# Optimization experiments

Measured on AMD Instinct MI355X. Metric: run time of the kernel, lower is better.

## Reference

```python
import jax, jax.numpy as jnp
import numpy as np

B, D, H, T = 8192, 256, 266, 20  # batch, dim, dim+10, num timesteps
LAMBDA = 1.0
SIGMA = 1.0
EPS = 1e-5  # torch BatchNorm1d default eps


def _bn(h, g, b):
    # training-mode BatchNorm1d: biased batch statistics over axis 0
    m = h.mean(0)
    v = h.var(0)
    return g * (h - m) * jax.lax.rsqrt(v + EPS) + b


def _hidden(x, W, b, g, be):
    return jax.nn.relu(_bn(x @ W.T + b, g, be))


def setup_inputs() -> dict:
    key = jax.random.key(0)
    ks = jax.random.split(key, 16)

    def n(k, shape, s=0.05):
        return jax.random.normal(k, shape, jnp.float32) * s

    inp = {}
    inp["x"] = jax.random.normal(ks[0], (B, D), jnp.float32)
    inp["xi"] = jax.random.normal(ks[1], (T, B, D), jnp.float32)
    inp["timegrid"] = jnp.linspace(0.0, 1.0, T + 1).astype(jnp.float32)
    # per-timestep stacks of Linear+BN params (i_h1, h1_h2, h2_o)
    inp["W1"] = n(ks[2], (T, H, D)); inp["b1"] = jnp.zeros((T, H), jnp.float32)
    inp["g1"] = jnp.ones((T, H), jnp.float32); inp["be1"] = jnp.zeros((T, H), jnp.float32)
    inp["W2"] = n(ks[3], (T, H, H)); inp["b2"] = jnp.zeros((T, H), jnp.float32)
    inp["g2"] = jnp.ones((T, H), jnp.float32); inp["be2"] = jnp.zeros((T, H), jnp.float32)
    inp["W3"] = n(ks[4], (T, D, H)); inp["b3"] = jnp.zeros((T, D), jnp.float32)
    # v0 network: hiddenLayer(D,H) -> hiddenLayer(H,H) -> hiddenLayer(H,1)
    inp["vW1"] = n(ks[5], (H, D)); inp["vb1"] = jnp.zeros((H,), jnp.float32)
    inp["vg1"] = jnp.ones((H,), jnp.float32); inp["vbe1"] = jnp.zeros((H,), jnp.float32)
    inp["vW2"] = n(ks[6], (H, H)); inp["vb2"] = jnp.zeros((H,), jnp.float32)
    inp["vg2"] = jnp.ones((H,), jnp.float32); inp["vbe2"] = jnp.zeros((H,), jnp.float32)
    inp["vW3"] = n(ks[7], (1, H)); inp["vb3"] = jnp.zeros((1,), jnp.float32)
    inp["vg3"] = jnp.ones((1,), jnp.float32); inp["vbe3"] = jnp.zeros((1,), jnp.float32)
    return inp


def reference(x, xi, timegrid, W1, b1, g1, be1, W2, b2, g2, be2, W3, b3,
              vW1, vb1, vg1, vbe1, vW2, vb2, vg2, vbe2, vW3, vb3, vg3, vbe3):
    # v0 sub-network evaluated on the initial x (i == 0 branch)
    v0 = _hidden(x, vW1, vb1, vg1, vbe1)
    v0 = _hidden(v0, vW2, vb2, vg2, vbe2)
    v0 = _hidden(v0, vW3, vb3, vg3, vbe3)  # [B, 1]

    hsteps = timegrid[1:] - timegrid[:-1]  # [T]

    def step(carry, inp_t):
        xt, vt = carry
        (W1t, b1t, g1t, be1t, W2t, b2t, g2t, be2t, W3t, b3t, ht, xit) = inp_t
        h1 = _hidden(xt, W1t, b1t, g1t, be1t)
        h2 = _hidden(h1, W2t, b2t, g2t, be2t)
        grad = h2 @ W3t.T + b3t                     # [B, D]
        alpha = -jnp.sqrt(LAMBDA) * grad
        f = jnp.sum(alpha * alpha, axis=1)          # ||alpha||_2^2 per row
        noise = SIGMA * jnp.sqrt(ht) * xit          # sigma*sqrt(h)*xi
        # diag(grad @ noise.T) == row-wise dot product (same math, O(B*D))
        dot = jnp.sum(grad * noise, axis=1)
        vt = vt - (f * ht)[:, None] + dot[:, None]
        xt = xt + alpha * ht + noise
        return (xt, vt), None

    (xT, vT), _ = jax.lax.scan(
        step, (x, v0),
        (W1, b1, g1, be1, W2, b2, g2, be2, W3, b3, hsteps, xi))
    return vT, xT
```

## Files before the change

### kernel.cpp

```cpp
#include <hip/hip_runtime.h>
#include <hip/hip_bf16.h>
#include <math.h>

#define BATCH 8192
#define DDIM 256
#define HDIM 266
#define NPAD 320
#define TSTEPS 20
#define BN_EPS 1e-5f
#define LSTR 72
#define NBLK 256
#define NBAR 64

typedef __attribute__((ext_vector_type(8))) short short8;
typedef __attribute__((ext_vector_type(4))) float f32x4;

__device__ __forceinline__ short f2bf(float f) {
    __hip_bfloat16 h = __float2bfloat16(f);
    return *reinterpret_cast<short*>(&h);
}
__device__ __forceinline__ float bf2f(short s) {
    union { unsigned u; float f; } v;
    v.u = ((unsigned)(unsigned short)s) << 16;
    return v.f;
}

#define SZ_W1B (20L * 320 * 256)
#define SZ_W2B (20L * 320 * 320)
#define SZ_W3B (20L * 256 * 320)
#define SZ_VW1 (320L * 256)
#define SZ_VW2 (320L * 320)
#define SZ_B1P (20L * 320)
#define SZ_B2P (20L * 320)
#define ZCOUNT (4L * 21 * NPAD + 2 + NBAR)
#define PREP_TOTAL (SZ_W1B + SZ_W2B + SZ_W3B + SZ_VW1 + SZ_VW2 + SZ_B1P + SZ_B2P + 3 * 320 + ZCOUNT)

__global__ __launch_bounds__(256)
void prep_k(short* __restrict__ W1b, const float* __restrict__ W1,
            short* __restrict__ W2b, const float* __restrict__ W2,
            short* __restrict__ W3b, const float* __restrict__ W3,
            short* __restrict__ vW1b, const float* __restrict__ vW1,
            short* __restrict__ vW2b, const float* __restrict__ vW2,
            float* __restrict__ b1p, const float* __restrict__ b1,
            float* __restrict__ b2p, const float* __restrict__ b2,
            float* __restrict__ vb1p, const float* __restrict__ vb1,
            float* __restrict__ vb2p, const float* __restrict__ vb2,
            float* __restrict__ vW3p, const float* __restrict__ vW3,
            float* __restrict__ zbase)
{
    long idx = (long)blockIdx.x * 256 + threadIdx.x;
    if (idx < SZ_W1B) {
        long k = idx % 256, r = (idx / 256) % 320, t = idx / (256L * 320);
        float v = (r < HDIM) ? W1[((size_t)t * HDIM + r) * 256 + k] : 0.0f;
        W1b[idx] = f2bf(v); return;
    }
    idx -= SZ_W1B;
    if (idx < SZ_W2B) {
        long k = idx % 320, r = (idx / 320) % 320, t = idx / (320L * 320);
        float v = (r < HDIM && k < HDIM) ? W2[((size_t)t * HDIM + r) * HDIM + k] : 0.0f;
        W2b[idx] = f2bf(v); return;
    }
    idx -= SZ_W2B;
    if (idx < SZ_W3B) {
        long k = idx % 320, r = (idx / 320) % 256, t = idx / (320L * 256);
        float v = (k < HDIM) ? W3[((size_t)t * 256 + r) * HDIM + k] : 0.0f;
        W3b[idx] = f2bf(v); return;
    }
    idx -= SZ_W3B;
    if (idx < SZ_VW1) {
        long k = idx % 256, r = idx / 256;
        float v = (r < HDIM) ? vW1[(size_t)r * 256 + k] : 0.0f;
        vW1b[idx] = f2bf(v); return;
    }
    idx -= SZ_VW1;
    if (idx < SZ_VW2) {
        long k = idx % 320, r = idx / 320;
        float v = (r < HDIM && k < HDIM) ? vW2[(size_t)r * HDIM + k] : 0.0f;
        vW2b[idx] = f2bf(v); return;
    }
    idx -= SZ_VW2;
    if (idx < SZ_B1P) { long n = idx % 320, t = idx / 320;
        b1p[idx] = (n < HDIM) ? b1[(size_t)t * HDIM + n] : 0.0f; return; }
    idx -= SZ_B1P;
    if (idx < SZ_B2P) { long n = idx % 320, t = idx / 320;
        b2p[idx] = (n < HDIM) ? b2[(size_t)t * HDIM + n] : 0.0f; return; }
    idx -= SZ_B2P;
    if (idx < 320) { vb1p[idx] = (idx < HDIM) ? vb1[idx] : 0.0f; return; }
    idx -= 320;
    if (idx < 320) { vb2p[idx] = (idx < HDIM) ? vb2[idx] : 0.0f; return; }
    idx -= 320;
    if (idx < 320) { vW3p[idx] = (idx < HDIM) ? vW3[idx] : 0.0f; return; }
    idx -= 320;
    if (idx < ZCOUNT) { zbase[idx] = 0.0f; return; }
}

__device__ __forceinline__ void gridbar(unsigned* __restrict__ bar, int idx, int tid)
{
    asm volatile("s_waitcnt vmcnt(0) lgkmcnt(0)" ::: "memory");
    __syncthreads();
    if (tid == 0) {
        __hip_atomic_fetch_add(&bar[idx], 1u, __ATOMIC_RELAXED, __HIP_MEMORY_SCOPE_AGENT);
        while (__hip_atomic_load(&bar[idx], __ATOMIC_RELAXED, __HIP_MEMORY_SCOPE_AGENT)
               < (unsigned)NBLK) {
            __builtin_amdgcn_s_sleep(2);
        }
    }
    __syncthreads();
}

__device__ __forceinline__ float aload(const float* p)
{
    return __hip_atomic_load(p, __ATOMIC_RELAXED, __HIP_MEMORY_SCOPE_AGENT);
}

__device__ __forceinline__ void bn_coeff(const float* __restrict__ cs,
                                         const float* __restrict__ cq,
                                         const float* __restrict__ g,
                                         const float* __restrict__ be,
                                         float* sS, float* sT, int tid)
{
    for (int k = tid; k < NPAD; k += 512) {
        float s = 0.0f, t = 0.0f;
        if (k < HDIM) {
            float mn = aload(&cs[k]) * (1.0f / BATCH);
            float vr = aload(&cq[k]) * (1.0f / BATCH) - mn * mn;
            float rs = rsqrtf(fmaxf(vr, 0.0f) + BN_EPS);
            s = g[k] * rs;
            t = be[k] - mn * s;
        }
        sS[k] = s; sT[k] = t;
    }
}

template<int NJ>
__device__ __forceinline__ void preload_w(const short* __restrict__ Wt, int KLEN,
                                          short8* rW, int tid)
{
    #pragma unroll
    for (int i = 0; i < NJ; ++i) {
        int s = tid + 512 * i;
        rW[i] = *(const short8*)(Wt + (size_t)(s >> 3) * KLEN + ((s & 7) * 8));
    }
}

template<int NKT, int NJ, bool BN>
__device__ __forceinline__ void gemm_phase(
    const short* __restrict__ Wt, const short* Asrc, short* As1, short* Bs,
    const float* sS, const float* sT, f32x4* acc, short8* rW, int tid)
{
    const int lane = tid & 63, q = lane >> 4, m = lane & 15;
    const int w = tid >> 6, rh = w >> 2, ch = w & 3;
    const int srowA = tid >> 3, kqA = (tid & 7) * 8;
    const int KLEN = NKT * 64;

    #pragma unroll
    for (int kt = 0; kt < NKT; ++kt) {
        if (BN) {
            if (tid < 256) {
                short8 v = *(const short8*)&Asrc[(kt * 32 + srowA) * LSTR + kqA];
                short8 ta;
                #pragma unroll
                for (int j = 0; j < 8; ++j) {
                    int k = kt * 64 + kqA + j;
                    float f = bf2f(v[j]);
                    f = fmaxf(f * sS[k] + sT[k], 0.0f);
                    ta[j] = f2bf(f);
                }
                *(short8*)&As1[srowA * LSTR + kqA] = ta;
            }
        }
        #pragma unroll
        for (int i = 0; i < NJ; ++i) {
            int s = tid + 512 * i;
            *(short8*)&Bs[(s >> 3) * LSTR + (s & 7) * 8] = rW[i];
        }
        __syncthreads();
        if (kt < NKT - 1) {
            #pragma unroll
            for (int i = 0; i < NJ; ++i) {
                int s = tid + 512 * i;
                rW[i] = *(const short8*)(Wt + (size_t)(s >> 3) * KLEN
                                         + (kt + 1) * 64 + ((s & 7) * 8));
            }
        }
        const short* ab = BN ? As1 : (Asrc + kt * 32 * LSTR);
        #pragma unroll
        for (int kk = 0; kk < 2; ++kk) {
            short8 fa = *(const short8*)&ab[(rh * 16 + m) * LSTR + kk * 32 + q * 8];
            #pragma unroll
            for (int j = 0; j < NJ; ++j) {
                short8 fb = *(const short8*)&Bs[(ch * (NJ * 16) + j * 16 + m) * LSTR
                                                + kk * 32 + q * 8];
                acc[j] = __builtin_amdgcn_mfma_f32_16x16x32_bf16(fa, fb, acc[j], 0, 0, 0);
            }
        }
        __syncthreads();
    }
}

__device__ __forceinline__ void epi_store_stats(
    const f32x4* acc, const float* __restrict__ bias, short* dst,
    float* redS, float* redQ, float* __restrict__ csum, float* __restrict__ csq,
    int tid)
{
    const int lane = tid & 63, q = lane >> 4, m = lane & 15;
    const int w = tid >> 6, rh = w >> 2, ch = w & 3;
    float csv[5], cqv[5];
    #pragma unroll
    for (int j = 0; j < 5; ++j) {
        const int col = ch * 80 + j * 16 + m;
        const float bv = bias[col];
        float s = 0.0f, sq = 0.0f;
        #pragma unroll
        for (int r = 0; r < 4; ++r) {
            float v = acc[j][r] + bv;
            int row = rh * 16 + q * 4 + r;
            dst[((col >> 6) * 32 + row) * LSTR + (col & 63)] = f2bf(v);
            s += v; sq += v * v;
        }
        csv[j] = s; cqv[j] = sq;
    }
    #pragma unroll
    for (int j = 0; j < 5; ++j) {
        csv[j] += __shfl_xor(csv[j], 16); csv[j] += __shfl_xor(csv[j], 32);
        cqv[j] += __shfl_xor(cqv[j], 16); cqv[j] += __shfl_xor(cqv[j], 32);
    }
    if (q == 0) {
        #pragma unroll
        for (int j = 0; j < 5; ++j) {
            int col = ch * 80 + j * 16 + m;
            redS[rh * NPAD + col] = csv[j];
            redQ[rh * NPAD + col] = cqv[j];
        }
    }
    __syncthreads();
    if (tid < HDIM) {
        atomicAdd(&csum[tid], redS[tid] + redS[NPAD + tid]);
        atomicAdd(&csq[tid],  redQ[tid] + redQ[NPAD + tid]);
    }
}

struct PArgs {
    const float* x; const float* xi; const float* tg;
    const short* W1b; const short* W2b; const short* W3b;
    const short* vW1b; const short* vW2b;
    const float* b1p; const float* b2p; const float* b3;
    const float* vb1p; const float* vb2p; const float* vW3p; const float* vb3;
    const float* g1; const float* be1; const float* g2; const float* be2;
    const float* vg1; const float* vbe1; const float* vg2; const float* vbe2;
    const float* vg3; const float* vbe3;
    float* csA; float* cqA; float* csB; float* cqB;
    float* s3; float* q3;
    unsigned* bars;
    float* out; float* xout;
};

__global__ __launch_bounds__(512)
void persist_k(PArgs p)
{
    __shared__ __align__(16) short xbuf[128 * LSTR];
    __shared__ __align__(16) short h1buf[160 * LSTR];
    __shared__ __align__(16) short h2buf[160 * LSTR];
    __shared__ __align__(16) short Bs[320 * LSTR];
    __shared__ __align__(16) short As1[32 * LSTR];
    __shared__ float sS[NPAD], sT[NPAD];
    __shared__ float redS[2 * NPAD], redQ[2 * NPAD];
    __shared__ float redF[128], redD[128];
    __shared__ float pre3L[32], vacc[32];

    const int tid = threadIdx.x;
    const int row0 = blockIdx.x * 32;
    const int lane = tid & 63, w = tid >> 6, q = lane >> 4, m = lane & 15;
    const int rh = w >> 2, ch = w & 3;
    int bidx = 0;

    for (int i2 = tid; i2 < 32 * 256; i2 += 512) {
        int row = i2 >> 8, col = i2 & 255;
        xbuf[((col >> 6) * 32 + row) * LSTR + (col & 63)] =
            f2bf(p.x[(size_t)(row0 + row) * DDIM + col]);
    }
    if (tid < 32) vacc[tid] = 0.0f;

    short8 rW[5];
    f32x4 acc[5];

    preload_w<5>(p.vW1b, DDIM, rW, tid);
    #pragma unroll
    for (int j = 0; j < 5; ++j) acc[j] = (f32x4){0.f, 0.f, 0.f, 0.f};
    __syncthreads();
    gemm_phase<4, 5, false>(p.vW1b, xbuf, As1, Bs, sS, sT, acc, rW, tid);
    epi_store_stats(acc, p.vb1p, h1buf, redS, redQ,
                    p.csA + 20 * NPAD, p.cqA + 20 * NPAD, tid);
    preload_w<5>(p.vW2b, NPAD, rW, tid);
    gridbar(p.bars, bidx++, tid);

    bn_coeff(p.csA + 20 * NPAD, p.cqA + 20 * NPAD, p.vg1, p.vbe1, sS, sT, tid);
    #pragma unroll
    for (int j = 0; j < 5; ++j) acc[j] = (f32x4){0.f, 0.f, 0.f, 0.f};
    __syncthreads();
    gemm_phase<5, 5, true>(p.vW2b, h1buf, As1, Bs, sS, sT, acc, rW, tid);
    epi_store_stats(acc, p.vb2p, h2buf, redS, redQ,
                    p.csB + 20 * NPAD, p.cqB + 20 * NPAD, tid);
    gridbar(p.bars, bidx++, tid);

    bn_coeff(p.csB + 20 * NPAD, p.cqB + 20 * NPAD, p.vg2, p.vbe2, sS, sT, tid);
    __syncthreads();
    {
        const int wv = tid >> 6, ln = tid & 63;
        float ps = 0.0f, pq = 0.0f;
        #pragma unroll
        for (int r4 = 0; r4 < 4; ++r4) {
            int row = wv * 4 + r4;
            float sum = 0.0f;
            #pragma unroll
            for (int c = 0; c < 5; ++c) {
                int k = c * 64 + ln;
                float v = fmaxf(bf2f(h2buf[(c * 32 + row) * LSTR + ln]) * sS[k] + sT[k], 0.0f);
                sum += v * p.vW3p[k];
            }
            sum += __shfl_xor(sum, 1);  sum += __shfl_xor(sum, 2);
            sum += __shfl_xor(sum, 4);  sum += __shfl_xor(sum, 8);
            sum += __shfl_xor(sum, 16); sum += __shfl_xor(sum, 32);
            if (ln == 0) {
                float pv = sum + p.vb3[0];
                pre3L[row] = pv;
                ps += pv; pq += pv * pv;
            }
        }
        if (ln == 0) { redF[wv] = ps; redD[wv] = pq; }
        __syncthreads();
        if (tid == 0) {
            float a = 0.0f, b = 0.0f;
            #pragma unroll
            for (int i = 0; i < 8; ++i) { a += redF[i]; b += redD[i]; }
            atomicAdd(p.s3, a); atomicAdd(p.q3, b);
        }
    }

    for (int t = 0; t < TSTEPS; ++t) {
        preload_w<5>(p.W1b + (size_t)t * NPAD * DDIM, DDIM, rW, tid);
        #pragma unroll
        for (int j = 0; j < 5; ++j) acc[j] = (f32x4){0.f, 0.f, 0.f, 0.f};
        gemm_phase<4, 5, false>(p.W1b + (size_t)t * NPAD * DDIM, xbuf, As1, Bs,
                                sS, sT, acc, rW, tid);
        epi_store_stats(acc, p.b1p + t * NPAD, h1buf, redS, redQ,
                        p.csA + t * NPAD, p.cqA + t * NPAD, tid);
        preload_w<5>(p.W2b + (size_t)t * NPAD * NPAD, NPAD, rW, tid);
        gridbar(p.bars, bidx++, tid);

        bn_coeff(p.csA + t * NPAD, p.cqA + t * NPAD,
                 p.g1 + (size_t)t * HDIM, p.be1 + (size_t)t * HDIM, sS, sT, tid);
        #pragma unroll
        for (int j = 0; j < 5; ++j) acc[j] = (f32x4){0.f, 0.f, 0.f, 0.f};
        __syncthreads();
        gemm_phase<5, 5, true>(p.W2b + (size_t)t * NPAD * NPAD, h1buf, As1, Bs,
                               sS, sT, acc, rW, tid);
        epi_store_stats(acc, p.b2p + t * NPAD, h2buf, redS, redQ,
                        p.csB + t * NPAD, p.cqB + t * NPAD, tid);
        preload_w<4>(p.W3b + (size_t)t * DDIM * NPAD, NPAD, rW, tid);
        gridbar(p.bars, bidx++, tid);

        bn_coeff(p.csB + t * NPAD, p.cqB + t * NPAD,
                 p.g2 + (size_t)t * HDIM, p.be2 + (size_t)t * HDIM, sS, sT, tid);
        __syncthreads();

        const float* xi_t = p.xi + (size_t)t * BATCH * DDIM;
        float xiv[16];
        #pragma unroll
        for (int j = 0; j < 4; ++j)
            #pragma unroll
            for (int r = 0; r < 4; ++r)
                xiv[j * 4 + r] = xi_t[(size_t)(row0 + rh * 16 + q * 4 + r) * DDIM
                                      + ch * 64 + j * 16 + m];

        #pragma unroll
        for (int j = 0; j < 4; ++j) acc[j] = (f32x4){0.f, 0.f, 0.f, 0.f};
        gemm_phase<5, 4, true>(p.W3b + (size_t)t * DDIM * NPAD, h2buf, As1, Bs,
                               sS, sT, acc, rW, tid);

        const float ht = p.tg[t + 1] - p.tg[t];
        const float sn = sqrtf(ht);
        float fr[4] = {0.f, 0.f, 0.f, 0.f};
        float dr[4] = {0.f, 0.f, 0.f, 0.f};
        #pragma unroll
        for (int j = 0; j < 4; ++j) {
            const int col = ch * 64 + j * 16 + m;
            const float bv = p.b3[(size_t)t * DDIM + col];
            #pragma unroll
            for (int r = 0; r < 4; ++r) {
                const int lr = rh * 16 + q * 4 + r;
                const size_t idx = (size_t)(row0 + lr) * DDIM + col;
                float grad = acc[j][r] + bv;
                float noise = sn * xiv[j * 4 + r];
                const int xo = (ch * 32 + lr) * LSTR + (j * 16 + m);
                float nx = bf2f(xbuf[xo]) - grad * ht + noise;
                xbuf[xo] = f2bf(nx);
                if (t == TSTEPS - 1) p.xout[idx] = nx;
                fr[r] += grad * grad;
                dr[r] += grad * noise;
            }
        }
        #pragma unroll
        for (int r = 0; r < 4; ++r) {
            fr[r] += __shfl_xor(fr[r], 1); dr[r] += __shfl_xor(dr[r], 1);
            fr[r] += __shfl_xor(fr[r], 2); dr[r] += __shfl_xor(dr[r], 2);
            fr[r] += __shfl_xor(fr[r], 4); dr[r] += __shfl_xor(dr[r], 4);
            fr[r] += __shfl_xor(fr[r], 8); dr[r] += __shfl_xor(dr[r], 8);
        }
        if (m == 0) {
            #pragma unroll
            for (int r = 0; r < 4; ++r) {
                redF[ch * 32 + rh * 16 + q * 4 + r] = fr[r];
                redD[ch * 32 + rh * 16 + q * 4 + r] = dr[r];
            }
        }
        __syncthreads();
        if (tid < 32) {
            float fsum = redF[tid] + redF[32 + tid] + redF[64 + tid] + redF[96 + tid];
            float dsum = redD[tid] + redD[32 + tid] + redD[64 + tid] + redD[96 + tid];
            vacc[tid] += dsum - fsum * ht;
        }
        __syncthreads();
    }

    if (tid < 32) {
        float mn = aload(p.s3) * (1.0f / BATCH);
        float va = fmaxf(aload(p.q3) * (1.0f / BATCH) - mn * mn, 0.0f);
        float rs = rsqrtf(va + BN_EPS);
        float v0 = fmaxf(p.vg3[0] * (pre3L[tid] - mn) * rs + p.vbe3[0], 0.0f);
        p.out[row0 + tid] = v0 + vacc[tid];
    }
}

extern "C" void kernel_launch(void* const* d_in, const int* in_sizes, int n_in,
                              void* d_out, int out_size, void* d_ws, size_t ws_size,
                              hipStream_t stream)
{
    const float* x    = (const float*)d_in[0];
    const float* xi   = (const float*)d_in[1];
    const float* tg   = (const float*)d_in[2];
    const float* W1   = (const float*)d_in[3];
    const float* b1   = (const float*)d_in[4];
    const float* g1   = (const float*)d_in[5];
    const float* be1  = (const float*)d_in[6];
    const float* W2   = (const float*)d_in[7];
    const float* b2   = (const float*)d_in[8];
    const float* g2   = (const float*)d_in[9];
    const float* be2  = (const float*)d_in[10];
    const float* W3   = (const float*)d_in[11];
    const float* b3   = (const float*)d_in[12];
    const float* vW1  = (const float*)d_in[13];
    const float* vb1  = (const float*)d_in[14];
    const float* vg1  = (const float*)d_in[15];
    const float* vbe1 = (const float*)d_in[16];
    const float* vW2  = (const float*)d_in[17];
    const float* vb2  = (const float*)d_in[18];
    const float* vg2  = (const float*)d_in[19];
    const float* vbe2 = (const float*)d_in[20];
    const float* vW3  = (const float*)d_in[21];
    const float* vb3  = (const float*)d_in[22];
    const float* vg3  = (const float*)d_in[23];
    const float* vbe3 = (const float*)d_in[24];

    float* out  = (float*)d_out;
    float* xout = out + BATCH;

    short* W1b  = (short*)d_ws;
    short* W2b  = W1b + SZ_W1B;
    short* W3b  = W2b + SZ_W2B;
    short* vW1b = W3b + SZ_W3B;
    short* vW2b = vW1b + SZ_VW1;
    float* b1p  = (float*)(vW2b + SZ_VW2);
    float* b2p  = b1p + TSTEPS * NPAD;
    float* vb1p = b2p + TSTEPS * NPAD;
    float* vb2p = vb1p + NPAD;
    float* vW3p = vb2p + NPAD;
    float* csA  = vW3p + NPAD;
    float* cqA  = csA + 21 * NPAD;
    float* csB  = cqA + 21 * NPAD;
    float* cqB  = csB + 21 * NPAD;
    float* s3   = cqB + 21 * NPAD;
    float* q3   = s3 + 1;
    unsigned* bars = (unsigned*)(q3 + 1);

    prep_k<<<dim3((int)((PREP_TOTAL + 255) / 256)), dim3(256), 0, stream>>>(
        W1b, W1, W2b, W2, W3b, W3, vW1b, vW1, vW2b, vW2,
        b1p, b1, b2p, b2, vb1p, vb1, vb2p, vb2, vW3p, vW3, csA);

    PArgs pa;
    pa.x = x; pa.xi = xi; pa.tg = tg;
    pa.W1b = W1b; pa.W2b = W2b; pa.W3b = W3b;
    pa.vW1b = vW1b; pa.vW2b = vW2b;
    pa.b1p = b1p; pa.b2p = b2p; pa.b3 = b3;
    pa.vb1p = vb1p; pa.vb2p = vb2p; pa.vW3p = vW3p; pa.vb3 = vb3;
    pa.g1 = g1; pa.be1 = be1; pa.g2 = g2; pa.be2 = be2;
    pa.vg1 = vg1; pa.vbe1 = vbe1; pa.vg2 = vg2; pa.vbe2 = vbe2;
    pa.vg3 = vg3; pa.vbe3 = vbe3;
    pa.csA = csA; pa.cqA = cqA; pa.csB = csB; pa.cqB = cqB;
    pa.s3 = s3; pa.q3 = q3;
    pa.bars = bars;
    pa.out = out; pa.xout = xout;

    void* kargs[] = { (void*)&pa };
    hipLaunchCooperativeKernel((const void*)persist_k, dim3(NBLK), dim3(512),
                               kargs, 0, stream);
}
```

Before: 1.193 ms.

## Spread BN stat atomics and grid barrier counters; load weights directly from global

Replaces the single-counter grid barrier with 16 sharded counters polled by one wavefront. BatchNorm column-stat atomics are spread across 8 copies that are summed when the coefficients are computed, which cuts atomic contention. The LDS-staged, K-tiled weight GEMM is replaced by MFMA B fragments loaded straight from global memory (L2), with the whole A tile prefetched into registers, removing per-k-tile syncthreads. The trade-off is more global and L2 load traffic, the loss of software prefetch for weights, and a later BN coefficient load for layer 3, which is now done after the barrier instead of overlapping with it.

```diff
diff --git a/kernel.cpp b/kernel.cpp
--- a/kernel.cpp
+++ b/kernel.cpp
@@ -10,6 +10,9 @@
 #define BN_EPS 1e-5f
 #define LSTR 72
 #define NBLK 256
+#define NTH 512
+#define NCPY 8
+#define NBARCNT 16
 #define NBAR 64
 
 typedef __attribute__((ext_vector_type(8))) short short8;
@@ -32,7 +35,7 @@
 #define SZ_VW2 (320L * 320)
 #define SZ_B1P (20L * 320)
 #define SZ_B2P (20L * 320)
-#define ZCOUNT (4L * 21 * NPAD + 2 + NBAR)
+#define ZCOUNT (4L * 21 * NCPY * NPAD + 2 * NCPY + NBAR * NBARCNT)
 #define PREP_TOTAL (SZ_W1B + SZ_W2B + SZ_W3B + SZ_VW1 + SZ_VW2 + SZ_B1P + SZ_B2P + 3 * 320 + ZCOUNT)
 
 __global__ __launch_bounds__(256)
@@ -94,15 +97,21 @@
     if (idx < ZCOUNT) { zbase[idx] = 0.0f; return; }
 }
 
-__device__ __forceinline__ void gridbar(unsigned* __restrict__ bar, int idx, int tid)
+__device__ __forceinline__ void gridbar(unsigned* __restrict__ bar, int idx,
+                                        int tid, int bid)
 {
     asm volatile("s_waitcnt vmcnt(0) lgkmcnt(0)" ::: "memory");
     __syncthreads();
-    if (tid == 0) {
-        __hip_atomic_fetch_add(&bar[idx], 1u, __ATOMIC_RELAXED, __HIP_MEMORY_SCOPE_AGENT);
-        while (__hip_atomic_load(&bar[idx], __ATOMIC_RELAXED, __HIP_MEMORY_SCOPE_AGENT)
-               < (unsigned)NBLK) {
-            __builtin_amdgcn_s_sleep(2);
+    if (tid == 0)
+        __hip_atomic_fetch_add(&bar[idx * NBARCNT + (bid & (NBARCNT - 1))], 1u,
+                               __ATOMIC_RELAXED, __HIP_MEMORY_SCOPE_AGENT);
+    if (tid < 64) {
+        const unsigned* c = &bar[idx * NBARCNT + (tid & (NBARCNT - 1))];
+        for (;;) {
+            unsigned v = __hip_atomic_load(c, __ATOMIC_RELAXED,
+                                           __HIP_MEMORY_SCOPE_AGENT);
+            if (__all(v >= (unsigned)(NBLK / NBARCNT))) break;
+            __builtin_amdgcn_s_sleep(1);
         }
     }
     __syncthreads();
@@ -113,17 +122,23 @@
     return __hip_atomic_load(p, __ATOMIC_RELAXED, __HIP_MEMORY_SCOPE_AGENT);
 }
 
-__device__ __forceinline__ void bn_coeff(const float* __restrict__ cs,
-                                         const float* __restrict__ cq,
-                                         const float* __restrict__ g,
-                                         const float* __restrict__ be,
-                                         float* sS, float* sT, int tid)
-{
-    for (int k = tid; k < NPAD; k += 512) {
+__device__ __forceinline__ void bn_coeff8(const float* __restrict__ cs,
+                                          const float* __restrict__ cq,
+                                          const float* __restrict__ g,
+                                          const float* __restrict__ be,
+                                          float* sS, float* sT, int tid)
+{
+    for (int k = tid; k < NPAD; k += NTH) {
         float s = 0.0f, t = 0.0f;
         if (k < HDIM) {
-            float mn = aload(&cs[k]) * (1.0f / BATCH);
-            float vr = aload(&cq[k]) * (1.0f / BATCH) - mn * mn;
+            float a = 0.0f, b = 0.0f;
+            #pragma unroll
+            for (int c = 0; c < NCPY; ++c) {
+                a += aload(&cs[c * NPAD + k]);
+                b += aload(&cq[c * NPAD + k]);
+            }
+            float mn = a * (1.0f / BATCH);
+            float vr = b * (1.0f / BATCH) - mn * mn;
             float rs = rsqrtf(fmaxf(vr, 0.0f) + BN_EPS);
             s = g[k] * rs;
             t = be[k] - mn * s;
@@ -132,80 +147,62 @@
     }
 }
 
-template<int NJ>
-__device__ __forceinline__ void preload_w(const short* __restrict__ Wt, int KLEN,
-                                          short8* rW, int tid)
-{
-    #pragma unroll
-    for (int i = 0; i < NJ; ++i) {
-        int s = tid + 512 * i;
-        rW[i] = *(const short8*)(Wt + (size_t)(s >> 3) * KLEN + ((s & 7) * 8));
-    }
-}
-
-template<int NKT, int NJ, bool BN>
-__device__ __forceinline__ void gemm_phase(
-    const short* __restrict__ Wt, const short* Asrc, short* As1, short* Bs,
-    const float* sS, const float* sT, f32x4* acc, short8* rW, int tid)
+template<int KS, int NJ, bool BN>
+__device__ __forceinline__ void gemm_direct(
+    const short* __restrict__ W, const short* Abuf, short* As1,
+    const float* sS, const float* sT, f32x4* acc, int tid)
 {
     const int lane = tid & 63, q = lane >> 4, m = lane & 15;
     const int w = tid >> 6, rh = w >> 2, ch = w & 3;
-    const int srowA = tid >> 3, kqA = (tid & 7) * 8;
-    const int KLEN = NKT * 64;
-
+
+    if (BN) {
+        const int NG = KS * 4;
+        for (int f = tid; f < 32 * NG; f += NTH) {
+            int kg = f % NG, row = f / NG;
+            int k = kg * 8;
+            int adr = ((k >> 6) * 32 + row) * LSTR + (k & 63);
+            short8 v = *(const short8*)&Abuf[adr];
+            short8 ta;
+            #pragma unroll
+            for (int j = 0; j < 8; ++j) {
+                float fx = bf2f(v[j]);
+                fx = fmaxf(fx * sS[k + j] + sT[k + j], 0.0f);
+                ta[j] = f2bf(fx);
+            }
+            *(short8*)&As1[adr] = ta;
+        }
+        __syncthreads();
+    }
+    const short* AB = BN ? As1 : Abuf;
+
+    short8 af[KS];
     #pragma unroll
-    for (int kt = 0; kt < NKT; ++kt) {
-        if (BN) {
-            if (tid < 256) {
-                short8 v = *(const short8*)&Asrc[(kt * 32 + srowA) * LSTR + kqA];
-                short8 ta;
-                #pragma unroll
-                for (int j = 0; j < 8; ++j) {
-                    int k = kt * 64 + kqA + j;
-                    float f = bf2f(v[j]);
-                    f = fmaxf(f * sS[k] + sT[k], 0.0f);
-                    ta[j] = f2bf(f);
-                }
-                *(short8*)&As1[srowA * LSTR + kqA] = ta;
-            }
-        }
-        #pragma unroll
-        for (int i = 0; i < NJ; ++i) {
-            int s = tid + 512 * i;
-            *(short8*)&Bs[(s >> 3) * LSTR + (s & 7) * 8] = rW[i];
-        }
-        __syncthreads();
-        if (kt < NKT - 1) {
-            #pragma unroll
-            for (int i = 0; i < NJ; ++i) {
-                int s = tid + 512 * i;
-                rW[i] = *(const short8*)(Wt + (size_t)(s >> 3) * KLEN
-                                         + (kt + 1) * 64 + ((s & 7) * 8));
-            }
-        }
-        const short* ab = BN ? As1 : (Asrc + kt * 32 * LSTR);
-        #pragma unroll
-        for (int kk = 0; kk < 2; ++kk) {
-            short8 fa = *(const short8*)&ab[(rh * 16 + m) * LSTR + kk * 32 + q * 8];
-            #pragma unroll
-            for (int j = 0; j < NJ; ++j) {
-                short8 fb = *(const short8*)&Bs[(ch * (NJ * 16) + j * 16 + m) * LSTR
-                                                + kk * 32 + q * 8];
-                acc[j] = __builtin_amdgcn_mfma_f32_16x16x32_bf16(fa, fb, acc[j], 0, 0, 0);
-            }
-        }
-        __syncthreads();
-    }
-}
-
-__device__ __forceinline__ void epi_store_stats(
-    const f32x4* acc, const float* __restrict__ bias, short* dst,
-    float* redS, float* redQ, float* __restrict__ csum, float* __restrict__ csq,
-    int tid)
+    for (int s = 0; s < KS; ++s)
+        af[s] = *(const short8*)&AB[((s >> 1) * 32 + rh * 16 + m) * LSTR
+                                    + (s & 1) * 32 + q * 8];
+    #pragma unroll
+    for (int j = 0; j < NJ; ++j) acc[j] = (f32x4){0.f, 0.f, 0.f, 0.f};
+
+    const int KLEN = KS * 32;
+    const short* wb = W + (size_t)(ch * (NJ * 16) + m) * KLEN + q * 8;
+    #pragma unroll
+    for (int s = 0; s < KS; ++s) {
+        short8 b[NJ];
+        #pragma unroll
+        for (int j = 0; j < NJ; ++j)
+            b[j] = *(const short8*)(wb + (size_t)j * 16 * KLEN + s * 32);
+        #pragma unroll
+        for (int j = 0; j < NJ; ++j)
+            acc[j] = __builtin_amdgcn_mfma_f32_16x16x32_bf16(af[s], b[j], acc[j], 0, 0, 0);
+    }
+}
+
+__device__ __forceinline__ void epi320(const f32x4* acc, const float* __restrict__ bias,
+                                       short* dst, float* __restrict__ cs,
+                                       float* __restrict__ cq, int tid, int bid)
 {
     const int lane = tid & 63, q = lane >> 4, m = lane & 15;
     const int w = tid >> 6, rh = w >> 2, ch = w & 3;
-    float csv[5], cqv[5];
     #pragma unroll
     for (int j = 0; j < 5; ++j) {
         const int col = ch * 80 + j * 16 + m;
@@ -218,25 +215,12 @@
             dst[((col >> 6) * 32 + row) * LSTR + (col & 63)] = f2bf(v);
             s += v; sq += v * v;
         }
-        csv[j] = s; cqv[j] = sq;
-    }
-    #pragma unroll
-    for (int j = 0; j < 5; ++j) {
-        csv[j] += __shfl_xor(csv[j], 16); csv[j] += __shfl_xor(csv[j], 32);
-        cqv[j] += __shfl_xor(cqv[j], 16); cqv[j] += __shfl_xor(cqv[j], 32);
-    }
-    if (q == 0) {
-        #pragma unroll
-        for (int j = 0; j < 5; ++j) {
-            int col = ch * 80 + j * 16 + m;
-            redS[rh * NPAD + col] = csv[j];
-            redQ[rh * NPAD + col] = cqv[j];
-        }
-    }
-    __syncthreads();
-    if (tid < HDIM) {
-        atomicAdd(&csum[tid], redS[tid] + redS[NPAD + tid]);
-        atomicAdd(&csq[tid],  redQ[tid] + redQ[NPAD + tid]);
+        s  += __shfl_xor(s, 16);  s  += __shfl_xor(s, 32);
+        sq += __shfl_xor(sq, 16); sq += __shfl_xor(sq, 32);
+        if (q == 0 && col < HDIM) {
+            atomicAdd(&cs[(bid & (NCPY - 1)) * NPAD + col], s);
+            atomicAdd(&cq[(bid & (NCPY - 1)) * NPAD + col], sq);
+        }
     }
 }
 
@@ -255,55 +239,49 @@
     float* out; float* xout;
 };
 
-__global__ __launch_bounds__(512)
+__global__ __launch_bounds__(NTH)
 void persist_k(PArgs p)
 {
-    __shared__ __align__(16) short xbuf[128 * LSTR];
-    __shared__ __align__(16) short h1buf[160 * LSTR];
-    __shared__ __align__(16) short h2buf[160 * LSTR];
-    __shared__ __align__(16) short Bs[320 * LSTR];
-    __shared__ __align__(16) short As1[32 * LSTR];
+    __shared__ __align__(16) short xbuf[4 * 32 * LSTR];
+    __shared__ __align__(16) short h1buf[5 * 32 * LSTR];
+    __shared__ __align__(16) short h2buf[5 * 32 * LSTR];
+    __shared__ __align__(16) short As1[5 * 32 * LSTR];
     __shared__ float sS[NPAD], sT[NPAD];
-    __shared__ float redS[2 * NPAD], redQ[2 * NPAD];
     __shared__ float redF[128], redD[128];
     __shared__ float pre3L[32], vacc[32];
 
     const int tid = threadIdx.x;
-    const int row0 = blockIdx.x * 32;
+    const int bid = blockIdx.x;
+    const int row0 = bid * 32;
     const int lane = tid & 63, w = tid >> 6, q = lane >> 4, m = lane & 15;
     const int rh = w >> 2, ch = w & 3;
     int bidx = 0;
 
-    for (int i2 = tid; i2 < 32 * 256; i2 += 512) {
+    for (int i2 = tid; i2 < 32 * 256; i2 += NTH) {
         int row = i2 >> 8, col = i2 & 255;
         xbuf[((col >> 6) * 32 + row) * LSTR + (col & 63)] =
             f2bf(p.x[(size_t)(row0 + row) * DDIM + col]);
     }
     if (tid < 32) vacc[tid] = 0.0f;
-
-    short8 rW[5];
+    __syncthreads();
+
     f32x4 acc[5];
 
-    preload_w<5>(p.vW1b, DDIM, rW, tid);
-    #pragma unroll
-    for (int j = 0; j < 5; ++j) acc[j] = (f32x4){0.f, 0.f, 0.f, 0.f};
+    gemm_direct<8, 5, false>(p.vW1b, xbuf, As1, sS, sT, acc, tid);
+    epi320(acc, p.vb1p, h1buf, p.csA + 20L * NCPY * NPAD, p.cqA + 20L * NCPY * NPAD,
+           tid, bid);
+    gridbar(p.bars, bidx++, tid, bid);
+
+    bn_coeff8(p.csA + 20L * NCPY * NPAD, p.cqA + 20L * NCPY * NPAD,
+              p.vg1, p.vbe1, sS, sT, tid);
     __syncthreads();
-    gemm_phase<4, 5, false>(p.vW1b, xbuf, As1, Bs, sS, sT, acc, rW, tid);
-    epi_store_stats(acc, p.vb1p, h1buf, redS, redQ,
-                    p.csA + 20 * NPAD, p.cqA + 20 * NPAD, tid);
-    preload_w<5>(p.vW2b, NPAD, rW, tid);
-    gridbar(p.bars, bidx++, tid);
-
-    bn_coeff(p.csA + 20 * NPAD, p.cqA + 20 * NPAD, p.vg1, p.vbe1, sS, sT, tid);
-    #pragma unroll
-    for (int j = 0; j < 5; ++j) acc[j] = (f32x4){0.f, 0.f, 0.f, 0.f};
-    __syncthreads();
-    gemm_phase<5, 5, true>(p.vW2b, h1buf, As1, Bs, sS, sT, acc, rW, tid);
-    epi_store_stats(acc, p.vb2p, h2buf, redS, redQ,
-                    p.csB + 20 * NPAD, p.cqB + 20 * NPAD, tid);
-    gridbar(p.bars, bidx++, tid);
-
-    bn_coeff(p.csB + 20 * NPAD, p.cqB + 20 * NPAD, p.vg2, p.vbe2, sS, sT, tid);
+    gemm_direct<10, 5, true>(p.vW2b, h1buf, As1, sS, sT, acc, tid);
+    epi320(acc, p.vb2p, h2buf, p.csB + 20L * NCPY * NPAD, p.cqB + 20L * NCPY * NPAD,
+           tid, bid);
+    gridbar(p.bars, bidx++, tid, bid);
+
+    bn_coeff8(p.csB + 20L * NCPY * NPAD, p.cqB + 20L * NCPY * NPAD,
+              p.vg2, p.vbe2, sS, sT, tid);
     __syncthreads();
     {
         const int wv = tid >> 6, ln = tid & 63;
@@ -315,7 +293,8 @@
             #pragma unroll
             for (int c = 0; c < 5; ++c) {
                 int k = c * 64 + ln;
-                float v = fmaxf(bf2f(h2buf[(c * 32 + row) * LSTR + ln]) * sS[k] + sT[k], 0.0f);
+                float v = fmaxf(bf2f(h2buf[(c * 32 + row) * LSTR + ln]) * sS[k] + sT[k],
+                                0.0f);
                 sum += v * p.vW3p[k];
             }
             sum += __shfl_xor(sum, 1);  sum += __shfl_xor(sum, 2);
@@ -333,36 +312,28 @@
             float a = 0.0f, b = 0.0f;
             #pragma unroll
             for (int i = 0; i < 8; ++i) { a += redF[i]; b += redD[i]; }
-            atomicAdd(p.s3, a); atomicAdd(p.q3, b);
+            atomicAdd(&p.s3[bid & (NCPY - 1)], a);
+            atomicAdd(&p.q3[bid & (NCPY - 1)], b);
         }
     }
 
     for (int t = 0; t < TSTEPS; ++t) {
-        preload_w<5>(p.W1b + (size_t)t * NPAD * DDIM, DDIM, rW, tid);
-        #pragma unroll
-        for (int j = 0; j < 5; ++j) acc[j] = (f32x4){0.f, 0.f, 0.f, 0.f};
-        gemm_phase<4, 5, false>(p.W1b + (size_t)t * NPAD * DDIM, xbuf, As1, Bs,
-                                sS, sT, acc, rW, tid);
-        epi_store_stats(acc, p.b1p + t * NPAD, h1buf, redS, redQ,
-                        p.csA + t * NPAD, p.cqA + t * NPAD, tid);
-        preload_w<5>(p.W2b + (size_t)t * NPAD * NPAD, NPAD, rW, tid);
-        gridbar(p.bars, bidx++, tid);
-
-        bn_coeff(p.csA + t * NPAD, p.cqA + t * NPAD,
-                 p.g1 + (size_t)t * HDIM, p.be1 + (size_t)t * HDIM, sS, sT, tid);
-        #pragma unroll
-        for (int j = 0; j < 5; ++j) acc[j] = (f32x4){0.f, 0.f, 0.f, 0.f};
-        __syncthreads();
-        gemm_phase<5, 5, true>(p.W2b + (size_t)t * NPAD * NPAD, h1buf, As1, Bs,
-                               sS, sT, acc, rW, tid);
-        epi_store_stats(acc, p.b2p + t * NPAD, h2buf, redS, redQ,
-                        p.csB + t * NPAD, p.cqB + t * NPAD, tid);
-        preload_w<4>(p.W3b + (size_t)t * DDIM * NPAD, NPAD, rW, tid);
-        gridbar(p.bars, bidx++, tid);
-
-        bn_coeff(p.csB + t * NPAD, p.cqB + t * NPAD,
-                 p.g2 + (size_t)t * HDIM, p.be2 + (size_t)t * HDIM, sS, sT, tid);
-        __syncthreads();
+        gemm_direct<8, 5, false>(p.W1b + (size_t)t * NPAD * DDIM, xbuf, As1,
+                                 sS, sT, acc, tid);
+        epi320(acc, p.b1p + t * NPAD, h1buf,
+               p.csA + (size_t)t * NCPY * NPAD, p.cqA + (size_t)t * NCPY * NPAD,
+               tid, bid);
+        gridbar(p.bars, bidx++, tid, bid);
+
+        bn_coeff8(p.csA + (size_t)t * NCPY * NPAD, p.cqA + (size_t)t * NCPY * NPAD,
+                  p.g1 + (size_t)t * HDIM, p.be1 + (size_t)t * HDIM, sS, sT, tid);
+        __syncthreads();
+        gemm_direct<10, 5, true>(p.W2b + (size_t)t * NPAD * NPAD, h1buf, As1,
+                                 sS, sT, acc, tid);
+        epi320(acc, p.b2p + t * NPAD, h2buf,
+               p.csB + (size_t)t * NCPY * NPAD, p.cqB + (size_t)t * NCPY * NPAD,
+               tid, bid);
+        gridbar(p.bars, bidx++, tid, bid);
 
         const float* xi_t = p.xi + (size_t)t * BATCH * DDIM;
         float xiv[16];
@@ -373,10 +344,11 @@
                 xiv[j * 4 + r] = xi_t[(size_t)(row0 + rh * 16 + q * 4 + r) * DDIM
                                       + ch * 64 + j * 16 + m];
 
-        #pragma unroll
-        for (int j = 0; j < 4; ++j) acc[j] = (f32x4){0.f, 0.f, 0.f, 0.f};
-        gemm_phase<5, 4, true>(p.W3b + (size_t)t * DDIM * NPAD, h2buf, As1, Bs,
-                               sS, sT, acc, rW, tid);
+        bn_coeff8(p.csB + (size_t)t * NCPY * NPAD, p.cqB + (size_t)t * NCPY * NPAD,
+                  p.g2 + (size_t)t * HDIM, p.be2 + (size_t)t * HDIM, sS, sT, tid);
+        __syncthreads();
+        gemm_direct<10, 4, true>(p.W3b + (size_t)t * DDIM * NPAD, h2buf, As1,
+                                 sS, sT, acc, tid);
 
         const float ht = p.tg[t + 1] - p.tg[t];
         const float sn = sqrtf(ht);
@@ -388,14 +360,14 @@
             const float bv = p.b3[(size_t)t * DDIM + col];
             #pragma unroll
             for (int r = 0; r < 4; ++r) {
-                const int lr = rh * 16 + q * 4 + r;
-                const size_t idx = (size_t)(row0 + lr) * DDIM + col;
+                const int row = rh * 16 + q * 4 + r;
                 float grad = acc[j][r] + bv;
                 float noise = sn * xiv[j * 4 + r];
-                const int xo = (ch * 32 + lr) * LSTR + (j * 16 + m);
+                const int xo = (ch * 32 + row) * LSTR + (j * 16 + m);
                 float nx = bf2f(xbuf[xo]) - grad * ht + noise;
                 xbuf[xo] = f2bf(nx);
-                if (t == TSTEPS - 1) p.xout[idx] = nx;
+                if (t == TSTEPS - 1)
+                    p.xout[(size_t)(row0 + row) * DDIM + col] = nx;
                 fr[r] += grad * grad;
                 dr[r] += grad * noise;
             }
@@ -424,8 +396,11 @@
     }
 
     if (tid < 32) {
-        float mn = aload(p.s3) * (1.0f / BATCH);
-        float va = fmaxf(aload(p.q3) * (1.0f / BATCH) - mn * mn, 0.0f);
+        float a = 0.0f, b = 0.0f;
+        #pragma unroll
+        for (int c = 0; c < NCPY; ++c) { a += aload(&p.s3[c]); b += aload(&p.q3[c]); }
+        float mn = a * (1.0f / BATCH);
+        float va = fmaxf(b * (1.0f / BATCH) - mn * mn, 0.0f);
         float rs = rsqrtf(va + BN_EPS);
         float v0 = fmaxf(p.vg3[0] * (pre3L[tid] - mn) * rs + p.vbe3[0], 0.0f);
         p.out[row0 + tid] = v0 + vacc[tid];
@@ -476,12 +451,12 @@
     float* vb2p = vb1p + NPAD;
     float* vW3p = vb2p + NPAD;
     float* csA  = vW3p + NPAD;
-    float* cqA  = csA + 21 * NPAD;
-    float* csB  = cqA + 21 * NPAD;
-    float* cqB  = csB + 21 * NPAD;
-    float* s3   = cqB + 21 * NPAD;
-    float* q3   = s3 + 1;
-    unsigned* bars = (unsigned*)(q3 + 1);
+    float* cqA  = csA + 21L * NCPY * NPAD;
+    float* csB  = cqA + 21L * NCPY * NPAD;
+    float* cqB  = csB + 21L * NCPY * NPAD;
+    float* s3   = cqB + 21L * NCPY * NPAD;
+    float* q3   = s3 + NCPY;
+    unsigned* bars = (unsigned*)(q3 + NCPY);
 
     prep_k<<<dim3((int)((PREP_TOTAL + 255) / 256)), dim3(256), 0, stream>>>(
         W1b, W1, W2b, W2, W3b, W3, vW1b, vW1, vW2b, vW2,
@@ -502,6 +477,6 @@
     pa.out = out; pa.xout = xout;
 
     void* kargs[] = { (void*)&pa };
-    hipLaunchCooperativeKernel((const void*)persist_k, dim3(NBLK), dim3(512),
+    hipLaunchCooperativeKernel((const void*)persist_k, dim3(NBLK), dim3(NTH),
                                kargs, 0, stream);
 }
```

Result: slower. 1.362 ms (+14.2%).
